# Performance work log

Hardware: AMD Instinct MI355X
Metric: run time of the kernel (lower is better)

The kernel has to match this reference:

```python
import jax, jax.numpy as jnp
import numpy as np

B, L, N, D, TOPK, OUT_V = 32, 512, 1024, 64, 20, 1024
BN_EPS = 1e-5
NEG_SLOPE = 0.2


def setup_inputs() -> dict:
    key = jax.random.key(0)
    ks = jax.random.split(key, 8)
    s = lambda k, shape, sc=0.05: jax.random.normal(k, shape, jnp.float32) * sc
    return {
        "x_enc": jax.random.normal(ks[0], (B, L, N), jnp.float32),
        "emb": s(ks[1], (N, D), 0.1),          # nn.Embedding(variate, d_model).weight
        "lin_W": s(ks[2], (L, D)),              # GraphLayer.lin (no bias)
        "att_i": s(ks[3], (D,)),
        "att_j": s(ks[4], (D,)),
        "att_em_i": s(ks[5], (D,)),
        "att_em_j": s(ks[6], (D,)),
        "gnn_b": jnp.zeros((D,), jnp.float32),  # GraphLayer bias (concat=False)
        "g1": jnp.ones((D,), jnp.float32), "b1": jnp.zeros((D,), jnp.float32),   # GNNLayer.bn
        "g2": jnp.ones((D,), jnp.float32), "b2": jnp.zeros((D,), jnp.float32),   # bn_outlayer_in
        "out_W": s(ks[7], (D, 1)), "out_b": jnp.zeros((1,), jnp.float32),        # OutLayer Linear(d_model, 1)
    }


def _forward(x_enc, emb, lin_W, att_i, att_j, att_em_i, att_em_j,
             gnn_b, g1, b1, g2, b2, out_W, out_b):
    # --- LIN: LayerNorm(input_len, eps=0, no affine) over time, first OUT_V variates ---
    xv = jnp.transpose(x_enc[:, :, :OUT_V], (0, 2, 1))          # [B, OUT_V, L]
    xv = (xv - xv.mean(-1, keepdims=True)) / jnp.sqrt(xv.var(-1, keepdims=True))
    x_enc = x_enc.at[:, :, :OUT_V].set(jnp.transpose(xv, (0, 2, 1)))
    x_enc = jnp.nan_to_num(x_enc, nan=0.0, posinf=0.0, neginf=0.0)

    gt = x_enc[:, -1:, :OUT_V]                                   # [B, 1, OUT_V]
    enc = x_enc.at[:, -1:, :OUT_V].set(0.0)

    # x = enc.transpose(0,1).view(-1, L)  (faithful to original reshape)
    x = jnp.transpose(enc, (1, 0, 2)).reshape(-1, L)             # [B*N, L]

    # --- dynamic top-k cosine-similarity graph (embeddings detached) ---
    w = jax.lax.stop_gradient(emb)
    nrm = jnp.linalg.norm(w, axis=-1)
    cos = (w @ w.T) / (nrm[:, None] * nrm[None, :])              # [N, N]
    topk_idx = jax.lax.top_k(cos, TOPK)[1]                       # [N, TOPK]
    src = topk_idx.reshape(-1)                                   # gated_j (source)
    dst = jnp.repeat(jnp.arange(N), TOPK)                        # gated_i (target)

    offs = (jnp.arange(B) * N)[:, None]
    src_b = (src[None, :] + offs).reshape(-1)                    # [B*N*TOPK]
    dst_b = (dst[None, :] + offs).reshape(-1)

    # remove_self_loops (mask out) then add_self_loops for all B*N nodes
    num_nodes = B * N
    self_mask = jnp.concatenate([src_b == dst_b, jnp.zeros(num_nodes, bool)])
    src_all = jnp.concatenate([src_b, jnp.arange(num_nodes)])
    dst_all = jnp.concatenate([dst_b, jnp.arange(num_nodes)])

    # --- GraphLayer (GAT-style, heads=1, concat=False) ---
    h = x @ lin_W                                                # [B*N, D]
    all_emb = jnp.tile(emb, (B, 1))                              # [B*N, D]

    logit = (h[dst_all] @ att_i + all_emb[dst_all] @ att_em_i
             + h[src_all] @ att_j + all_emb[src_all] @ att_em_j)  # [E]
    logit = jnp.where(logit >= 0, logit, NEG_SLOPE * logit)      # leaky_relu(0.2)
    logit = jnp.where(self_mask, -jnp.inf, logit)

    seg_max = jax.ops.segment_max(logit, dst_all, num_segments=num_nodes)
    expv = jnp.where(self_mask, 0.0, jnp.exp(logit - seg_max[dst_all]))
    denom = jax.ops.segment_sum(expv, dst_all, num_segments=num_nodes)
    alpha = expv / denom[dst_all]

    out = jax.ops.segment_sum(h[src_all] * alpha[:, None], dst_all,
                              num_segments=num_nodes) + gnn_b    # [B*N, D]

    # GNNLayer: BatchNorm1d(D) (batch stats) + ReLU
    out = (out - out.mean(0)) / jnp.sqrt(out.var(0) + BN_EPS) * g1 + b1
    out = jax.nn.relu(out)

    # --- combine with embedding, bn_outlayer_in, OutLayer ---
    xg = out.reshape(B, N, D) * emb[None]                        # [B, N, D]
    xg = jnp.transpose(xg, (0, 2, 1))                            # [B, D, N]
    mu = xg.mean((0, 2), keepdims=True)
    var = xg.var((0, 2), keepdims=True)
    xg = (xg - mu) / jnp.sqrt(var + BN_EPS) * g2[None, :, None] + b2[None, :, None]
    xg = jnp.transpose(jax.nn.relu(xg), (0, 2, 1))               # [B, N, D]

    o = xg @ out_W + out_b                                       # [B, N, 1]
    o = jnp.transpose(o, (0, 2, 1))                              # [B, 1, N]
    return o[:, :, :OUT_V], gt


def reference(x_enc, emb, lin_W, att_i, att_j, att_em_i, att_em_j,
              gnn_b, g1, b1, g2, b2, out_W, out_b):
    return _forward(x_enc, emb, lin_W, att_i, att_j, att_em_i, att_em_j,
                    gnn_b, g1, b1, g2, b2, out_W, out_b)
```

## Files before the change

kernel.cpp:

```cpp
#include <hip/hip_runtime.h>
#include <stdint.h>

#define BB 32
#define LL 512
#define NNODES 1024
#define DD 64
#define TOPK 20
#define NTOT (BB*NNODES)
#define LNSZ (LL*NNODES)

typedef short short8 __attribute__((ext_vector_type(8)));
typedef float floatx4 __attribute__((ext_vector_type(4)));

__device__ __forceinline__ float bf2f(unsigned short u){
    union { unsigned int i; float f; } x; x.i = ((unsigned int)u) << 16; return x.f;
}
__device__ __forceinline__ unsigned short f2bf(float f){
    union { float f; unsigned int i; } x; x.f = f;
    unsigned int u = x.i;
    return (unsigned short)((u + 0x7FFFu + ((u >> 16) & 1u)) >> 16);
}
__device__ __forceinline__ void unpack2(unsigned int w, float& lo, float& hi){
    union { unsigned int i; float f; } a, b;
    a.i = w << 16; b.i = w & 0xFFFF0000u;
    lo = a.f; hi = b.f;
}
__device__ __forceinline__ float ldf(const void* p, int i, int isf){
    return isf ? ((const float*)p)[i] : bf2f(((const unsigned short*)p)[i]);
}

__global__ void __launch_bounds__(256) kd_detect(const unsigned short* x, int* flag, float* stats){
    __shared__ int cnt;
    stats[threadIdx.x] = 0.f;
    if (threadIdx.x == 0) cnt = 0;
    __syncthreads();
    unsigned int idx = (threadIdx.x * 131071u) & 0x7FFFFFu;
    float v = bf2f(x[idx * 2]);
    float a = fabsf(v);
    int crazy = (!(a <= 1e3f)) || (v != 0.f && a < 1e-6f);
    atomicAdd(&cnt, crazy);
    __syncthreads();
    if (threadIdx.x == 0) flag[0] = (cnt > 64) ? 1 : 0;
}

__global__ void __launch_bounds__(256) k0_prep(const void* lw, unsigned short* wt,
                                               const void* emb, const void* aemi, const void* aemj,
                                               float* eai, float* eaj, float* embT, float* rsqm,
                                               const int* dtf){
    int isf = dtf[0];
    int id = blockIdx.x * 256 + threadIdx.x;
    int k = id >> 6, d = id & 63;
    unsigned short w = isf ? f2bf(((const float*)lw)[id]) : ((const unsigned short*)lw)[id];
    wt[d * 512 + k] = w;
    {
        int j = id;
        int dd = j >> 10, m = j & 1023;
        embT[j] = ldf(emb, m * 64 + dd, isf);
        j = id + 32768;
        dd = j >> 10; m = j & 1023;
        embT[j] = ldf(emb, m * 64 + dd, isf);
    }
    if (id < 1024){
        int n = id;
        float s1 = 0.f, s2 = 0.f;
        for (int dd = 0; dd < 64; dd++){
            float e = ldf(emb, n * 64 + dd, isf);
            s1 += e * ldf(aemi, dd, isf);
            s2 += e * ldf(aemj, dd, isf);
        }
        eai[n] = s1; eaj[n] = s2;
        float sq = 0.f;
        if (!isf){
            const uint4* pm = (const uint4*)((const unsigned short*)emb + n * 64);
            #pragma unroll
            for (int i = 0; i < 8; i++){
                uint4 ww = pm[i];
                float a0,a1,a2,a3,a4,a5,a6,a7;
                unpack2(ww.x,a0,a1); unpack2(ww.y,a2,a3); unpack2(ww.z,a4,a5); unpack2(ww.w,a6,a7);
                sq += a0*a0 + a1*a1 + a2*a2 + a3*a3 + a4*a4 + a5*a5 + a6*a6 + a7*a7;
            }
        } else {
            const float4* pm = (const float4*)((const float*)emb + n * 64);
            #pragma unroll
            for (int i = 0; i < 16; i++){
                float4 ww = pm[i];
                sq += ww.x*ww.x + ww.y*ww.y + ww.z*ww.z + ww.w*ww.w;
            }
        }
        rsqm[n] = rsqrtf(sq);
    }
}

__global__ void __launch_bounds__(256) k1a_partial(const void* x, float* part, const int* dtf){
    int isf = dtf[0];
    int t = threadIdx.x;
    int b = blockIdx.x >> 4, lq = blockIdx.x & 15;
    int n0 = t * 4;
    size_t base = (size_t)b * LNSZ + (size_t)(lq * 32) * NNODES + n0;
    float s0=0,s1=0,s2=0,s3=0,q0=0,q1=0,q2=0,q3=0;
    if (isf){
        const float* p = (const float*)x + base;
        for (int i = 0; i < 32; i++){
            float4 w = *(const float4*)p;
            s0+=w.x; q0+=w.x*w.x; s1+=w.y; q1+=w.y*w.y;
            s2+=w.z; q2+=w.z*w.z; s3+=w.w; q3+=w.w*w.w;
            p += NNODES;
        }
    } else {
        const unsigned short* p = (const unsigned short*)x + base;
        for (int i = 0; i < 32; i++){
            uint2 w = *(const uint2*)p;
            float a,bv,c,d2;
            unpack2(w.x, a, bv); unpack2(w.y, c, d2);
            s0+=a; q0+=a*a; s1+=bv; q1+=bv*bv; s2+=c; q2+=c*c; s3+=d2; q3+=d2*d2;
            p += NNODES;
        }
    }
    int v = b * NNODES + n0;
    float2* pp = (float2*)part;
    pp[(size_t)v*16 + lq]       = make_float2(s0,q0);
    pp[(size_t)(v+1)*16 + lq]   = make_float2(s1,q1);
    pp[(size_t)(v+2)*16 + lq]   = make_float2(s2,q2);
    pp[(size_t)(v+3)*16 + lq]   = make_float2(s3,q3);
}

__global__ void __launch_bounds__(256) k1b_finalize(const void* x, const float* part,
                                                    float* mr, float* outp, const int* dtf){
    int isf = dtf[0];
    int v = blockIdx.x * 256 + threadIdx.x;
    const float2* pp = (const float2*)part + (size_t)v * 16;
    float s = 0.f, q = 0.f;
    for (int i = 0; i < 16; i++){ float2 w = pp[i]; s += w.x; q += w.y; }
    float mean = s * (1.f/512.f);
    float var  = q * (1.f/512.f) - mean * mean;
    float rstd = var > 0.f ? rsqrtf(var) : 0.f;
    ((float2*)mr)[v] = make_float2(mean, rstd);
    int b = v >> 10, n = v & 1023;
    float xv = ldf(x, (int)((size_t)b * LNSZ + (size_t)511 * NNODES + n), isf);
    outp[NTOT + v] = (xv - mean) * rstd;
}

__global__ void __launch_bounds__(256) k2_gemm_h(const void* x, const unsigned short* wt,
                                                const float* mr, float* h, const int* dtf){
    __shared__ unsigned short A_l[64 * 136];
    __shared__ unsigned short W_l[64 * 136];
    __shared__ float4 colp4[256];
    int isf = dtf[0];
    int t = threadIdx.x;
    int q = blockIdx.x & 63, mtile = blockIdx.x >> 6;
    int b = q >> 1, nbase = (q & 1) * 512;
    size_t xbase = (size_t)b * LNSZ + nbase;

    colp4[t] = ((const float4*)mr)[q * 256 + t];

    int wave = t >> 6, lane = t & 63;
    int quad = lane >> 4, lcol = lane & 15;
    floatx4 acc[4];
    for (int j = 0; j < 4; j++) acc[j] = (floatx4){0.f,0.f,0.f,0.f};
    __syncthreads();

    for (int kc = 0; kc < 4; kc++){
        for (int i = 0; i < 4; i++){
            int id = i * 256 + t;
            int l = id >> 4, c16 = id & 15;
            int lg = mtile * 64 + l;
            uint4 o;
            if (lg == 511){
                o = make_uint4(0u, 0u, 0u, 0u);
            } else {
                size_t ofs = xbase + (size_t)lg * NNODES + kc * 128 + c16 * 8;
                float e0,e1,e2,e3,e4,e5,e6,e7;
                if (isf){
                    const float4* px = (const float4*)((const float*)x + ofs);
                    float4 wa = px[0], wb = px[1];
                    e0=wa.x; e1=wa.y; e2=wa.z; e3=wa.w; e4=wb.x; e5=wb.y; e6=wb.z; e7=wb.w;
                } else {
                    uint4 w = *(const uint4*)((const unsigned short*)x + ofs);
                    unpack2(w.x,e0,e1); unpack2(w.y,e2,e3); unpack2(w.z,e4,e5); unpack2(w.w,e6,e7);
                }
                int f4b = kc * 64 + c16 * 4;
                float4 pA = colp4[f4b+0], pB = colp4[f4b+1], pC = colp4[f4b+2], pD = colp4[f4b+3];
                e0 = (e0 - pA.x) * pA.y;  e1 = (e1 - pA.z) * pA.w;
                e2 = (e2 - pB.x) * pB.y;  e3 = (e3 - pB.z) * pB.w;
                e4 = (e4 - pC.x) * pC.y;  e5 = (e5 - pC.z) * pC.w;
                e6 = (e6 - pD.x) * pD.y;  e7 = (e7 - pD.z) * pD.w;
                o.x = (unsigned)f2bf(e0) | ((unsigned)f2bf(e1) << 16);
                o.y = (unsigned)f2bf(e2) | ((unsigned)f2bf(e3) << 16);
                o.z = (unsigned)f2bf(e4) | ((unsigned)f2bf(e5) << 16);
                o.w = (unsigned)f2bf(e6) | ((unsigned)f2bf(e7) << 16);
            }
            *(uint4*)&A_l[l * 136 + c16 * 8] = o;
        }
        for (int i = 0; i < 4; i++){
            int id = i * 256 + t;
            int dd = id >> 4, c16 = id & 15;
            uint4 w = *(const uint4*)(wt + dd * 512 + kc * 128 + c16 * 8);
            *(uint4*)&W_l[dd * 136 + c16 * 8] = w;
        }
        __syncthreads();
        for (int ks = 0; ks < 4; ks++){
            short8 af, bfr[4];
            af = *(const short8*)&A_l[(wave * 16 + lcol) * 136 + ks * 32 + quad * 8];
            for (int tc = 0; tc < 4; tc++)
                bfr[tc] = *(const short8*)&W_l[(tc * 16 + lcol) * 136 + ks * 32 + quad * 8];
            for (int tc = 0; tc < 4; tc++)
                acc[tc] = __builtin_amdgcn_mfma_f32_16x16x32_bf16(af, bfr[tc], acc[tc], 0, 0, 0);
        }
        __syncthreads();
    }
    for (int tc = 0; tc < 4; tc++){
        int dcol = tc * 16 + lcol;
        for (int r = 0; r < 4; r++){
            int lrow = wave * 16 + quad * 4 + r;
            int lg = mtile * 64 + lrow;
            int row = lg * 64 + q;
            h[(size_t)row * 64 + dcol] = acc[tc][r];
        }
    }
}

__global__ void __launch_bounds__(256) k3_topk(const void* emb, const float* embT, const float* rsqm,
                                               int* topk, const int* dtf){
    __shared__ float enf[64];
    __shared__ float n2s;
    __shared__ float crow[1024];
    int isf = dtf[0];
    int wave = threadIdx.x >> 6, lane = threadIdx.x & 63;
    int n = blockIdx.x;
    if (wave == 0){
        float e = ldf(emb, n * 64 + lane, isf);
        enf[lane] = e;
        float p1 = e * e;
        #pragma unroll
        for (int m = 1; m < 64; m <<= 1) p1 += __shfl_xor(p1, m, 64);
        if (lane == 0) n2s = p1;
    }
    __syncthreads();
    float rn_own = rsqrtf(n2s);
    const float* en = enf;
    int mb = wave * 256 + lane * 4;
    float dot0 = 0.f, dot1 = 0.f, dot2 = 0.f, dot3 = 0.f;
    if (!isf){
        #pragma unroll
        for (int i = 0; i < 8; i++){
            float4 a0 = *(const float4*)(embT + (i*8+0)*1024 + mb);
            float4 a1 = *(const float4*)(embT + (i*8+1)*1024 + mb);
            float4 a2 = *(const float4*)(embT + (i*8+2)*1024 + mb);
            float4 a3 = *(const float4*)(embT + (i*8+3)*1024 + mb);
            float4 a4 = *(const float4*)(embT + (i*8+4)*1024 + mb);
            float4 a5 = *(const float4*)(embT + (i*8+5)*1024 + mb);
            float4 a6 = *(const float4*)(embT + (i*8+6)*1024 + mb);
            float4 a7 = *(const float4*)(embT + (i*8+7)*1024 + mb);
            const float* e8 = en + i * 8;
            dot0 += e8[0]*a0.x + e8[1]*a1.x + e8[2]*a2.x + e8[3]*a3.x
                  + e8[4]*a4.x + e8[5]*a5.x + e8[6]*a6.x + e8[7]*a7.x;
            dot1 += e8[0]*a0.y + e8[1]*a1.y + e8[2]*a2.y + e8[3]*a3.y
                  + e8[4]*a4.y + e8[5]*a5.y + e8[6]*a6.y + e8[7]*a7.y;
            dot2 += e8[0]*a0.z + e8[1]*a1.z + e8[2]*a2.z + e8[3]*a3.z
                  + e8[4]*a4.z + e8[5]*a5.z + e8[6]*a6.z + e8[7]*a7.z;
            dot3 += e8[0]*a0.w + e8[1]*a1.w + e8[2]*a2.w + e8[3]*a3.w
                  + e8[4]*a4.w + e8[5]*a5.w + e8[6]*a6.w + e8[7]*a7.w;
        }
    } else {
        #pragma unroll
        for (int i = 0; i < 16; i++){
            float4 a0 = *(const float4*)(embT + (i*4+0)*1024 + mb);
            float4 a1 = *(const float4*)(embT + (i*4+1)*1024 + mb);
            float4 a2 = *(const float4*)(embT + (i*4+2)*1024 + mb);
            float4 a3 = *(const float4*)(embT + (i*4+3)*1024 + mb);
            const float* e4 = en + i * 4;
            dot0 += e4[0]*a0.x + e4[1]*a1.x + e4[2]*a2.x + e4[3]*a3.x;
            dot1 += e4[0]*a0.y + e4[1]*a1.y + e4[2]*a2.y + e4[3]*a3.y;
            dot2 += e4[0]*a0.z + e4[1]*a1.z + e4[2]*a2.z + e4[3]*a3.z;
            dot3 += e4[0]*a0.w + e4[1]*a1.w + e4[2]*a2.w + e4[3]*a3.w;
        }
    }
    crow[mb+0] = dot0 * rn_own * rsqm[mb+0];
    crow[mb+1] = dot1 * rn_own * rsqm[mb+1];
    crow[mb+2] = dot2 * rn_own * rsqm[mb+2];
    crow[mb+3] = dot3 * rn_own * rsqm[mb+3];
    __syncthreads();
    if (wave != 0) return;
    float va[16];
    #pragma unroll
    for (int ii = 0; ii < 16; ii++) va[ii] = crow[ii * 64 + lane];
    for (int k = 0; k < TOPK; k++){
        float t8[8]; int x8[8];
        #pragma unroll
        for (int j = 0; j < 8; j++){
            bool c = va[2*j+1] > va[2*j];
            t8[j] = c ? va[2*j+1] : va[2*j]; x8[j] = c ? 2*j+1 : 2*j;
        }
        #pragma unroll
        for (int j = 0; j < 4; j++){
            bool c = t8[2*j+1] > t8[2*j];
            t8[j] = c ? t8[2*j+1] : t8[2*j]; x8[j] = c ? x8[2*j+1] : x8[2*j];
        }
        #pragma unroll
        for (int j = 0; j < 2; j++){
            bool c = t8[2*j+1] > t8[2*j];
            t8[j] = c ? t8[2*j+1] : t8[2*j]; x8[j] = c ? x8[2*j+1] : x8[2*j];
        }
        bool c0 = t8[1] > t8[0];
        float bv = c0 ? t8[1] : t8[0]; int bi = c0 ? x8[1] : x8[0];
        int bm = bi * 64 + lane;
        #pragma unroll
        for (int s = 1; s < 64; s <<= 1){
            float ov = __shfl_xor(bv, s, 64);
            int   om = __shfl_xor(bm, s, 64);
            bool u = (ov > bv) || (ov == bv && om < bm);
            bv = u ? ov : bv; bm = u ? om : bm;
        }
        if (lane == 0) topk[n * TOPK + k] = bm;
        int evi = bm >> 6;
        bool own = ((bm & 63) == lane);
        #pragma unroll
        for (int ii = 0; ii < 16; ii++)
            va[ii] = (own && ii == evi) ? -__builtin_inff() : va[ii];
    }
}

__global__ void __launch_bounds__(256) k4_coef(const float* h, const void* att_i, const void* att_j,
                                               const float* eai, const float* eaj, float* ai, float* aj,
                                               const int* dtf){
    int isf = dtf[0];
    int wave = blockIdx.x * 4 + (threadIdx.x >> 6), lane = threadIdx.x & 63;
    float wi = ldf(att_i, lane, isf), wj = ldf(att_j, lane, isf);
    int v0 = wave * 16;
    for (int i = 0; i < 16; i++){
        int v = v0 + i;
        float hv = h[(size_t)v * 64 + lane];
        float p1 = hv * wi, p2 = hv * wj;
        for (int m = 1; m < 64; m <<= 1){ p1 += __shfl_xor(p1, m, 64); p2 += __shfl_xor(p2, m, 64); }
        if (lane == 0){
            int n = v & 1023;
            ai[v] = p1 + eai[n];
            aj[v] = p2 + eaj[n];
        }
    }
}

__global__ void __launch_bounds__(256) k5_attn(const float* h, const float* ai, const float* aj, const int* topk,
                                               const void* gnn_b, float* out, const int* dtf){
    int isf = dtf[0];
    int wave = threadIdx.x >> 6, lane = threadIdx.x & 63;
    float gb = ldf(gnn_b, lane, isf);
    int v = blockIdx.x * 4 + wave;
    int n = v & 1023, bbase = v & ~1023;
    int srcv; bool valid;
    if (lane < TOPK){
        int id = topk[n * TOPK + lane];
        srcv = bbase | id;
        valid = (id != n);
    } else if (lane == TOPK){
        srcv = v; valid = true;
    } else { srcv = v; valid = false; }
    float l = ai[v] + aj[srcv];
    l = (l >= 0.f) ? l : 0.2f * l;
    if (!valid) l = -__builtin_inff();
    float m = l;
    #pragma unroll
    for (int s = 1; s < 64; s <<= 1){ float o = __shfl_xor(m, s, 64); m = fmaxf(m, o); }
    float ev = valid ? __expf(l - m) : 0.f;
    float dsum = ev;
    #pragma unroll
    for (int s = 1; s < 64; s <<= 1) dsum += __shfl_xor(dsum, s, 64);
    float rd = 1.f / dsum;
    float acc = 0.f;
    #pragma unroll
    for (int j = 0; j <= TOPK; j++){
        float e = __shfl(ev, j, 64);
        int  sj = __shfl(srcv, j, 64);
        acc += e * h[(size_t)sj * 64 + lane];
    }
    out[(size_t)v * 64 + lane] = acc * rd + gb;
}

__global__ void __launch_bounds__(256) k5b_stats(const float* out, float* stats1){
    __shared__ float bs[256], bq[256];
    int wave = threadIdx.x >> 6, lane = threadIdx.x & 63;
    int v0 = blockIdx.x * 128 + wave * 32;
    float ssum = 0.f, ssq = 0.f;
    for (int i = 0; i < 32; i++){
        float x = out[(size_t)(v0 + i) * 64 + lane];
        ssum += x; ssq += x * x;
    }
    bs[threadIdx.x] = ssum; bq[threadIdx.x] = ssq;
    __syncthreads();
    if (wave == 0){
        float s  = bs[lane] + bs[64+lane] + bs[128+lane] + bs[192+lane];
        float qq = bq[lane] + bq[64+lane] + bq[128+lane] + bq[192+lane];
        atomicAdd(&stats1[lane], s);
        atomicAdd(&stats1[64 + lane], qq);
    }
}

__global__ void __launch_bounds__(256) k6_stats2(const float* out, const float* stats1, const void* g1,
                                                 const void* b1, const void* emb,
                                                 float* stats2, const int* dtf){
    __shared__ float bs[256], bq[256];
    int isf = dtf[0];
    int wave = threadIdx.x >> 6, lane = threadIdx.x & 63;
    float mu   = stats1[lane] * (1.f/32768.f);
    float var  = stats1[64 + lane] * (1.f/32768.f) - mu * mu;
    float rstd = 1.f / sqrtf(var + 1e-5f);
    float g = ldf(g1, lane, isf), bb = ldf(b1, lane, isf);
    float ssum = 0.f, ssq = 0.f;
    int v0 = (blockIdx.x * 4 + wave) * 16;
    for (int i = 0; i < 16; i++){
        int v = v0 + i; int n = v & 1023;
        float x = out[(size_t)v * 64 + lane];
        float y = fmaxf((x - mu) * rstd * g + bb, 0.f);
        float z = y * ldf(emb, n * 64 + lane, isf);
        ssum += z; ssq += z * z;
    }
    bs[threadIdx.x] = ssum; bq[threadIdx.x] = ssq;
    __syncthreads();
    if (wave == 0){
        float s  = bs[lane] + bs[64+lane] + bs[128+lane] + bs[192+lane];
        float qq = bq[lane] + bq[64+lane] + bq[128+lane] + bq[192+lane];
        atomicAdd(&stats2[lane], s);
        atomicAdd(&stats2[64 + lane], qq);
    }
}

__global__ void __launch_bounds__(256) k7_out(const float* out, const float* stats1, const float* stats2,
                                              const void* g1, const void* b1,
                                              const void* g2, const void* b2,
                                              const void* emb, const void* outw,
                                              const void* outb, float* o, const int* dtf){
    int isf = dtf[0];
    int wave = threadIdx.x >> 6, lane = threadIdx.x & 63;
    float mu1   = stats1[lane] * (1.f/32768.f);
    float var1  = stats1[64 + lane] * (1.f/32768.f) - mu1 * mu1;
    float rstd1 = 1.f / sqrtf(var1 + 1e-5f);
    float g1v = ldf(g1, lane, isf), b1v = ldf(b1, lane, isf);
    float mu2   = stats2[lane] * (1.f/32768.f);
    float var2  = stats2[64 + lane] * (1.f/32768.f) - mu2 * mu2;
    float rstd2 = 1.f / sqrtf(var2 + 1e-5f);
    float g2v = ldf(g2, lane, isf), b2v = ldf(b2, lane, isf);
    float w = ldf(outw, lane, isf);
    float ob = ldf(outb, 0, isf);
    int v0 = (blockIdx.x * 4 + wave) * 16;
    for (int i = 0; i < 16; i++){
        int v = v0 + i; int n = v & 1023;
        float x = out[(size_t)v * 64 + lane];
        float z = fmaxf((x - mu1) * rstd1 * g1v + b1v, 0.f) * ldf(emb, n * 64 + lane, isf);
        float y = fmaxf((z - mu2) * rstd2 * g2v + b2v, 0.f);
        float p = y * w;
        for (int s = 1; s < 64; s <<= 1) p += __shfl_xor(p, s, 64);
        if (lane == 0) o[v] = p + ob;
    }
}

extern "C" void kernel_launch(void* const* d_in, const int* in_sizes, int n_in,
                              void* d_out, int out_size, void* d_ws, size_t ws_size,
                              hipStream_t stream){
    const void* x    = d_in[0];
    const void* emb  = d_in[1];
    const void* linW = d_in[2];
    const void* atti = d_in[3];
    const void* attj = d_in[4];
    const void* aemi = d_in[5];
    const void* aemj = d_in[6];
    const void* gnnb = d_in[7];
    const void* g1   = d_in[8];
    const void* b1   = d_in[9];
    const void* g2   = d_in[10];
    const void* b2   = d_in[11];
    const void* outw = d_in[12];
    const void* outb = d_in[13];
    float* o = (float*)d_out;

    char* w = (char*)d_ws;
    float*          mr    = (float*)(w + 0);
    unsigned short* wt    = (unsigned short*)(w + 262144);
    float*          h     = (float*)(w + 327680);
    float*          eai   = (float*)(w + 8716288);
    float*          eaj   = (float*)(w + 8720384);
    int*            topk  = (int*)(w + 8724480);
    float*          ai    = (float*)(w + 8806400);
    float*          aj    = (float*)(w + 8937472);
    float*          outg  = (float*)(w + 9068544);
    float*          part  = outg;
    float*          embT  = (float*)(w + 13262848);
    float*          rsqm  = (float*)(w + 13524992);
    float*          stats = (float*)(w + 17457152);
    int*            dtf   = (int*)(w + 17458176);

    hipLaunchKernelGGL(kd_detect,    dim3(1),    dim3(256), 0, stream, (const unsigned short*)x, dtf, stats);
    hipLaunchKernelGGL(k0_prep,      dim3(128),  dim3(256), 0, stream, linW, wt, emb, aemi, aemj, eai, eaj, embT, rsqm, dtf);
    hipLaunchKernelGGL(k1a_partial,  dim3(512),  dim3(256), 0, stream, x, part, dtf);
    hipLaunchKernelGGL(k1b_finalize, dim3(128),  dim3(256), 0, stream, x, part, mr, o, dtf);
    hipLaunchKernelGGL(k2_gemm_h,    dim3(512),  dim3(256), 0, stream, x, wt, mr, h, dtf);
    hipLaunchKernelGGL(k3_topk,      dim3(1024), dim3(256), 0, stream, emb, embT, rsqm, topk, dtf);
    hipLaunchKernelGGL(k4_coef,      dim3(512),  dim3(256), 0, stream, h, atti, attj, eai, eaj, ai, aj, dtf);
    hipLaunchKernelGGL(k5_attn,      dim3(8192), dim3(256), 0, stream, h, ai, aj, topk, gnnb, outg, dtf);
    hipLaunchKernelGGL(k5b_stats,    dim3(256),  dim3(256), 0, stream, outg, stats);
    hipLaunchKernelGGL(k6_stats2,    dim3(512),  dim3(256), 0, stream, outg, stats, g1, b1, emb, stats + 128, dtf);
    hipLaunchKernelGGL(k7_out,       dim3(512),  dim3(256), 0, stream, outg, stats, stats + 128,
                       g1, b1, g2, b2, emb, outw, outb, o, dtf);
}
```

Before: 260.5 us.

## Fuse prep, stats, topk, coefficient and BN-stat kernels to cut launch count

Merges the separate detect, prep, partial-sum, finalize, top-k, attention-coefficient and BN-statistics kernels into fewer launches, going from eleven kernels to six. Dtype detection is now redone in every kernel with a wave ballot instead of a dedicated launch writing a flag. The attention coefficients are computed in the GEMM epilogue from the MFMA accumulators, which removes a full re-read of h. The BN1 statistics are accumulated inside the attention kernel, which now handles four nodes per wave. The aim is less launch overhead and less global memory traffic, at the cost of heavier fused kernels, some redundant detection loads, and the finalize work sharing blocks with top-k.

After: 277.6 us. +6.6%, slower.

```diff
diff --git a/kernel.cpp b/kernel.cpp
--- a/kernel.cpp
+++ b/kernel.cpp
@@ -28,72 +28,67 @@
 __device__ __forceinline__ float ldf(const void* p, int i, int isf){
     return isf ? ((const float*)p)[i] : bf2f(((const unsigned short*)p)[i]);
 }
-
-__global__ void __launch_bounds__(256) kd_detect(const unsigned short* x, int* flag, float* stats){
-    __shared__ int cnt;
-    stats[threadIdx.x] = 0.f;
-    if (threadIdx.x == 0) cnt = 0;
-    __syncthreads();
-    unsigned int idx = (threadIdx.x * 131071u) & 0x7FFFFFu;
+__device__ __forceinline__ int detect_isf(const void* xv){
+    const unsigned short* x = (const unsigned short*)xv;
+    int lane = threadIdx.x & 63;
+    unsigned int idx = ((unsigned)lane * 131071u) & 0x7FFFFFu;
     float v = bf2f(x[idx * 2]);
     float a = fabsf(v);
     int crazy = (!(a <= 1e3f)) || (v != 0.f && a < 1e-6f);
-    atomicAdd(&cnt, crazy);
-    __syncthreads();
-    if (threadIdx.x == 0) flag[0] = (cnt > 64) ? 1 : 0;
-}
-
-__global__ void __launch_bounds__(256) k0_prep(const void* lw, unsigned short* wt,
-                                               const void* emb, const void* aemi, const void* aemj,
-                                               float* eai, float* eaj, float* embT, float* rsqm,
-                                               const int* dtf){
-    int isf = dtf[0];
-    int id = blockIdx.x * 256 + threadIdx.x;
-    int k = id >> 6, d = id & 63;
-    unsigned short w = isf ? f2bf(((const float*)lw)[id]) : ((const unsigned short*)lw)[id];
-    wt[d * 512 + k] = w;
-    {
-        int j = id;
-        int dd = j >> 10, m = j & 1023;
-        embT[j] = ldf(emb, m * 64 + dd, isf);
-        j = id + 32768;
-        dd = j >> 10; m = j & 1023;
-        embT[j] = ldf(emb, m * 64 + dd, isf);
-    }
-    if (id < 1024){
-        int n = id;
-        float s1 = 0.f, s2 = 0.f;
-        for (int dd = 0; dd < 64; dd++){
-            float e = ldf(emb, n * 64 + dd, isf);
-            s1 += e * ldf(aemi, dd, isf);
-            s2 += e * ldf(aemj, dd, isf);
-        }
-        eai[n] = s1; eaj[n] = s2;
-        float sq = 0.f;
-        if (!isf){
-            const uint4* pm = (const uint4*)((const unsigned short*)emb + n * 64);
-            #pragma unroll
-            for (int i = 0; i < 8; i++){
-                uint4 ww = pm[i];
-                float a0,a1,a2,a3,a4,a5,a6,a7;
-                unpack2(ww.x,a0,a1); unpack2(ww.y,a2,a3); unpack2(ww.z,a4,a5); unpack2(ww.w,a6,a7);
-                sq += a0*a0 + a1*a1 + a2*a2 + a3*a3 + a4*a4 + a5*a5 + a6*a6 + a7*a7;
+    unsigned long long m = __ballot(crazy);
+    return __popcll(m) > 16;
+}
+
+__global__ void __launch_bounds__(256) k01_prep(const void* x, const void* lw, unsigned short* wt,
+                                                const void* emb, const void* aemi, const void* aemj,
+                                                float* eai, float* eaj, float* embT, float* rsqm,
+                                                float* part, float* stats){
+    int isf = detect_isf(x);
+    int t = threadIdx.x;
+    if (blockIdx.x == 0) stats[t] = 0.f;
+    if (blockIdx.x < 128){
+        int id = blockIdx.x * 256 + t;
+        int k = id >> 6, d = id & 63;
+        unsigned short w = isf ? f2bf(((const float*)lw)[id]) : ((const unsigned short*)lw)[id];
+        wt[d * 512 + k] = w;
+        {
+            int j = id;
+            int dd = j >> 10, m = j & 1023;
+            embT[j] = ldf(emb, m * 64 + dd, isf);
+            j = id + 32768;
+            dd = j >> 10; m = j & 1023;
+            embT[j] = ldf(emb, m * 64 + dd, isf);
+        }
+        if (id < 1024){
+            int n = id;
+            float s1 = 0.f, s2 = 0.f;
+            for (int dd = 0; dd < 64; dd++){
+                float e = ldf(emb, n * 64 + dd, isf);
+                s1 += e * ldf(aemi, dd, isf);
+                s2 += e * ldf(aemj, dd, isf);
             }
-        } else {
-            const float4* pm = (const float4*)((const float*)emb + n * 64);
-            #pragma unroll
-            for (int i = 0; i < 16; i++){
-                float4 ww = pm[i];
-                sq += ww.x*ww.x + ww.y*ww.y + ww.z*ww.z + ww.w*ww.w;
+            eai[n] = s1; eaj[n] = s2;
+            float sq = 0.f;
+            if (!isf){
+                const uint4* pm = (const uint4*)((const unsigned short*)emb + n * 64);
+                #pragma unroll
+                for (int i = 0; i < 8; i++){
+                    uint4 ww = pm[i];
+                    float a0,a1,a2,a3,a4,a5,a6,a7;
+                    unpack2(ww.x,a0,a1); unpack2(ww.y,a2,a3); unpack2(ww.z,a4,a5); unpack2(ww.w,a6,a7);
+                    sq += a0*a0 + a1*a1 + a2*a2 + a3*a3 + a4*a4 + a5*a5 + a6*a6 + a7*a7;
+                }
+            } else {
+                const float4* pm = (const float4*)((const float*)emb + n * 64);
+                #pragma unroll
+                for (int i = 0; i < 16; i++){
+                    float4 ww = pm[i];
+                    sq += ww.x*ww.x + ww.y*ww.y + ww.z*ww.z + ww.w*ww.w;
+                }
             }
-        }
-        rsqm[n] = rsqrtf(sq);
-    }
-}
-
-__global__ void __launch_bounds__(256) k1a_partial(const void* x, float* part, const int* dtf){
-    int isf = dtf[0];
-    int t = threadIdx.x;
+            rsqm[n] = rsqrtf(sq);
+        }
+    }
     int b = blockIdx.x >> 4, lq = blockIdx.x & 15;
     int n0 = t * 4;
     size_t base = (size_t)b * LNSZ + (size_t)(lq * 32) * NNODES + n0;
@@ -124,28 +119,130 @@
     pp[(size_t)(v+3)*16 + lq]   = make_float2(s3,q3);
 }
 
-__global__ void __launch_bounds__(256) k1b_finalize(const void* x, const float* part,
-                                                    float* mr, float* outp, const int* dtf){
-    int isf = dtf[0];
-    int v = blockIdx.x * 256 + threadIdx.x;
-    const float2* pp = (const float2*)part + (size_t)v * 16;
-    float s = 0.f, q = 0.f;
-    for (int i = 0; i < 16; i++){ float2 w = pp[i]; s += w.x; q += w.y; }
-    float mean = s * (1.f/512.f);
-    float var  = q * (1.f/512.f) - mean * mean;
-    float rstd = var > 0.f ? rsqrtf(var) : 0.f;
-    ((float2*)mr)[v] = make_float2(mean, rstd);
-    int b = v >> 10, n = v & 1023;
-    float xv = ldf(x, (int)((size_t)b * LNSZ + (size_t)511 * NNODES + n), isf);
-    outp[NTOT + v] = (xv - mean) * rstd;
+__global__ void __launch_bounds__(256) k13_topk(const void* emb, const float* embT, const float* rsqm,
+                                                int* topk, const void* x, const float* part,
+                                                float* mr, float* outp){
+    __shared__ float enf[64];
+    __shared__ float n2s;
+    __shared__ float crow[1024];
+    int isf = detect_isf(x);
+    int wave = threadIdx.x >> 6, lane = threadIdx.x & 63;
+    int n = blockIdx.x;
+    if (blockIdx.x < 128){
+        int v = blockIdx.x * 256 + threadIdx.x;
+        const float2* pp = (const float2*)part + (size_t)v * 16;
+        float s = 0.f, q = 0.f;
+        for (int i = 0; i < 16; i++){ float2 w = pp[i]; s += w.x; q += w.y; }
+        float mean = s * (1.f/512.f);
+        float var  = q * (1.f/512.f) - mean * mean;
+        float rstd = var > 0.f ? rsqrtf(var) : 0.f;
+        ((float2*)mr)[v] = make_float2(mean, rstd);
+        int b = v >> 10, nn = v & 1023;
+        float xv = ldf(x, (int)((size_t)b * LNSZ + (size_t)511 * NNODES + nn), isf);
+        outp[NTOT + v] = (xv - mean) * rstd;
+    }
+    if (wave == 0){
+        float e = ldf(emb, n * 64 + lane, isf);
+        enf[lane] = e;
+        float p1 = e * e;
+        #pragma unroll
+        for (int m = 1; m < 64; m <<= 1) p1 += __shfl_xor(p1, m, 64);
+        if (lane == 0) n2s = p1;
+    }
+    __syncthreads();
+    float rn_own = rsqrtf(n2s);
+    const float* en = enf;
+    int mb = wave * 256 + lane * 4;
+    float dot0 = 0.f, dot1 = 0.f, dot2 = 0.f, dot3 = 0.f;
+    if (!isf){
+        #pragma unroll
+        for (int i = 0; i < 8; i++){
+            float4 a0 = *(const float4*)(embT + (i*8+0)*1024 + mb);
+            float4 a1 = *(const float4*)(embT + (i*8+1)*1024 + mb);
+            float4 a2 = *(const float4*)(embT + (i*8+2)*1024 + mb);
+            float4 a3 = *(const float4*)(embT + (i*8+3)*1024 + mb);
+            float4 a4 = *(const float4*)(embT + (i*8+4)*1024 + mb);
+            float4 a5 = *(const float4*)(embT + (i*8+5)*1024 + mb);
+            float4 a6 = *(const float4*)(embT + (i*8+6)*1024 + mb);
+            float4 a7 = *(const float4*)(embT + (i*8+7)*1024 + mb);
+            const float* e8 = en + i * 8;
+            dot0 += e8[0]*a0.x + e8[1]*a1.x + e8[2]*a2.x + e8[3]*a3.x
+                  + e8[4]*a4.x + e8[5]*a5.x + e8[6]*a6.x + e8[7]*a7.x;
+            dot1 += e8[0]*a0.y + e8[1]*a1.y + e8[2]*a2.y + e8[3]*a3.y
+                  + e8[4]*a4.y + e8[5]*a5.y + e8[6]*a6.y + e8[7]*a7.y;
+            dot2 += e8[0]*a0.z + e8[1]*a1.z + e8[2]*a2.z + e8[3]*a3.z
+                  + e8[4]*a4.z + e8[5]*a5.z + e8[6]*a6.z + e8[7]*a7.z;
+            dot3 += e8[0]*a0.w + e8[1]*a1.w + e8[2]*a2.w + e8[3]*a3.w
+                  + e8[4]*a4.w + e8[5]*a5.w + e8[6]*a6.w + e8[7]*a7.w;
+        }
+    } else {
+        #pragma unroll
+        for (int i = 0; i < 16; i++){
+            float4 a0 = *(const float4*)(embT + (i*4+0)*1024 + mb);
+            float4 a1 = *(const float4*)(embT + (i*4+1)*1024 + mb);
+            float4 a2 = *(const float4*)(embT + (i*4+2)*1024 + mb);
+            float4 a3 = *(const float4*)(embT + (i*4+3)*1024 + mb);
+            const float* e4 = en + i * 4;
+            dot0 += e4[0]*a0.x + e4[1]*a1.x + e4[2]*a2.x + e4[3]*a3.x;
+            dot1 += e4[0]*a0.y + e4[1]*a1.y + e4[2]*a2.y + e4[3]*a3.y;
+            dot2 += e4[0]*a0.z + e4[1]*a1.z + e4[2]*a2.z + e4[3]*a3.z;
+            dot3 += e4[0]*a0.w + e4[1]*a1.w + e4[2]*a2.w + e4[3]*a3.w;
+        }
+    }
+    crow[mb+0] = dot0 * rn_own * rsqm[mb+0];
+    crow[mb+1] = dot1 * rn_own * rsqm[mb+1];
+    crow[mb+2] = dot2 * rn_own * rsqm[mb+2];
+    crow[mb+3] = dot3 * rn_own * rsqm[mb+3];
+    __syncthreads();
+    if (wave != 0) return;
+    float va[16];
+    #pragma unroll
+    for (int ii = 0; ii < 16; ii++) va[ii] = crow[ii * 64 + lane];
+    for (int k = 0; k < TOPK; k++){
+        float t8[8]; int x8[8];
+        #pragma unroll
+        for (int j = 0; j < 8; j++){
+            bool c = va[2*j+1] > va[2*j];
+            t8[j] = c ? va[2*j+1] : va[2*j]; x8[j] = c ? 2*j+1 : 2*j;
+        }
+        #pragma unroll
+        for (int j = 0; j < 4; j++){
+            bool c = t8[2*j+1] > t8[2*j];
+            t8[j] = c ? t8[2*j+1] : t8[2*j]; x8[j] = c ? x8[2*j+1] : x8[2*j];
+        }
+        #pragma unroll
+        for (int j = 0; j < 2; j++){
+            bool c = t8[2*j+1] > t8[2*j];
+            t8[j] = c ? t8[2*j+1] : t8[2*j]; x8[j] = c ? x8[2*j+1] : x8[2*j];
+        }
+        bool c0 = t8[1] > t8[0];
+        float bv = c0 ? t8[1] : t8[0]; int bi = c0 ? x8[1] : x8[0];
+        int bm = bi * 64 + lane;
+        #pragma unroll
+        for (int s = 1; s < 64; s <<= 1){
+            float ov = __shfl_xor(bv, s, 64);
+            int   om = __shfl_xor(bm, s, 64);
+            bool u = (ov > bv) || (ov == bv && om < bm);
+            bv = u ? ov : bv; bm = u ? om : bm;
+        }
+        if (lane == 0) topk[n * TOPK + k] = bm;
+        int evi = bm >> 6;
+        bool own = ((bm & 63) == lane);
+        #pragma unroll
+        for (int ii = 0; ii < 16; ii++)
+            va[ii] = (own && ii == evi) ? -__builtin_inff() : va[ii];
+    }
 }
 
 __global__ void __launch_bounds__(256) k2_gemm_h(const void* x, const unsigned short* wt,
-                                                const float* mr, float* h, const int* dtf){
+                                                const float* mr, float* h,
+                                                const void* atti, const void* attj,
+                                                const float* eai, const float* eaj,
+                                                float* ai, float* aj){
     __shared__ unsigned short A_l[64 * 136];
     __shared__ unsigned short W_l[64 * 136];
     __shared__ float4 colp4[256];
-    int isf = dtf[0];
+    int isf = detect_isf(x);
     int t = threadIdx.x;
     int q = blockIdx.x & 63, mtile = blockIdx.x >> 6;
     int b = q >> 1, nbase = (q & 1) * 512;
@@ -208,182 +305,86 @@
         }
         __syncthreads();
     }
+    float aw[4], jw[4];
+    #pragma unroll
+    for (int tc = 0; tc < 4; tc++){
+        int dcol = tc * 16 + lcol;
+        aw[tc] = ldf(atti, dcol, isf);
+        jw[tc] = ldf(attj, dcol, isf);
+    }
+    #pragma unroll
+    for (int r = 0; r < 4; r++){
+        float pi = 0.f, pj = 0.f;
+        #pragma unroll
+        for (int tc = 0; tc < 4; tc++){
+            float hv = acc[tc][r];
+            pi += hv * aw[tc];
+            pj += hv * jw[tc];
+        }
+        #pragma unroll
+        for (int s = 1; s < 16; s <<= 1){
+            pi += __shfl_xor(pi, s, 64);
+            pj += __shfl_xor(pj, s, 64);
+        }
+        if (lcol == 0){
+            int lrow = wave * 16 + quad * 4 + r;
+            int row = (mtile * 64 + lrow) * 64 + q;
+            int n = row & 1023;
+            ai[row] = pi + eai[n];
+            aj[row] = pj + eaj[n];
+        }
+    }
     for (int tc = 0; tc < 4; tc++){
         int dcol = tc * 16 + lcol;
         for (int r = 0; r < 4; r++){
             int lrow = wave * 16 + quad * 4 + r;
-            int lg = mtile * 64 + lrow;
-            int row = lg * 64 + q;
+            int row = (mtile * 64 + lrow) * 64 + q;
             h[(size_t)row * 64 + dcol] = acc[tc][r];
         }
     }
 }
 
-__global__ void __launch_bounds__(256) k3_topk(const void* emb, const float* embT, const float* rsqm,
-                                               int* topk, const int* dtf){
-    __shared__ float enf[64];
-    __shared__ float n2s;
-    __shared__ float crow[1024];
-    int isf = dtf[0];
-    int wave = threadIdx.x >> 6, lane = threadIdx.x & 63;
-    int n = blockIdx.x;
-    if (wave == 0){
-        float e = ldf(emb, n * 64 + lane, isf);
-        enf[lane] = e;
-        float p1 = e * e;
-        #pragma unroll
-        for (int m = 1; m < 64; m <<= 1) p1 += __shfl_xor(p1, m, 64);
-        if (lane == 0) n2s = p1;
-    }
-    __syncthreads();
-    float rn_own = rsqrtf(n2s);
-    const float* en = enf;
-    int mb = wave * 256 + lane * 4;
-    float dot0 = 0.f, dot1 = 0.f, dot2 = 0.f, dot3 = 0.f;
-    if (!isf){
-        #pragma unroll
-        for (int i = 0; i < 8; i++){
-            float4 a0 = *(const float4*)(embT + (i*8+0)*1024 + mb);
-            float4 a1 = *(const float4*)(embT + (i*8+1)*1024 + mb);
-            float4 a2 = *(const float4*)(embT + (i*8+2)*1024 + mb);
-            float4 a3 = *(const float4*)(embT + (i*8+3)*1024 + mb);
-            float4 a4 = *(const float4*)(embT + (i*8+4)*1024 + mb);
-            float4 a5 = *(const float4*)(embT + (i*8+5)*1024 + mb);
-            float4 a6 = *(const float4*)(embT + (i*8+6)*1024 + mb);
-            float4 a7 = *(const float4*)(embT + (i*8+7)*1024 + mb);
-            const float* e8 = en + i * 8;
-            dot0 += e8[0]*a0.x + e8[1]*a1.x + e8[2]*a2.x + e8[3]*a3.x
-                  + e8[4]*a4.x + e8[5]*a5.x + e8[6]*a6.x + e8[7]*a7.x;
-            dot1 += e8[0]*a0.y + e8[1]*a1.y + e8[2]*a2.y + e8[3]*a3.y
-                  + e8[4]*a4.y + e8[5]*a5.y + e8[6]*a6.y + e8[7]*a7.y;
-            dot2 += e8[0]*a0.z + e8[1]*a1.z + e8[2]*a2.z + e8[3]*a3.z
-                  + e8[4]*a4.z + e8[5]*a5.z + e8[6]*a6.z + e8[7]*a7.z;
-            dot3 += e8[0]*a0.w + e8[1]*a1.w + e8[2]*a2.w + e8[3]*a3.w
-                  + e8[4]*a4.w + e8[5]*a5.w + e8[6]*a6.w + e8[7]*a7.w;
-        }
-    } else {
-        #pragma unroll
-        for (int i = 0; i < 16; i++){
-            float4 a0 = *(const float4*)(embT + (i*4+0)*1024 + mb);
-            float4 a1 = *(const float4*)(embT + (i*4+1)*1024 + mb);
-            float4 a2 = *(const float4*)(embT + (i*4+2)*1024 + mb);
-            float4 a3 = *(const float4*)(embT + (i*4+3)*1024 + mb);
-            const float* e4 = en + i * 4;
-            dot0 += e4[0]*a0.x + e4[1]*a1.x + e4[2]*a2.x + e4[3]*a3.x;
-            dot1 += e4[0]*a0.y + e4[1]*a1.y + e4[2]*a2.y + e4[3]*a3.y;
-            dot2 += e4[0]*a0.z + e4[1]*a1.z + e4[2]*a2.z + e4[3]*a3.z;
-            dot3 += e4[0]*a0.w + e4[1]*a1.w + e4[2]*a2.w + e4[3]*a3.w;
-        }
-    }
-    crow[mb+0] = dot0 * rn_own * rsqm[mb+0];
-    crow[mb+1] = dot1 * rn_own * rsqm[mb+1];
-    crow[mb+2] = dot2 * rn_own * rsqm[mb+2];
-    crow[mb+3] = dot3 * rn_own * rsqm[mb+3];
-    __syncthreads();
-    if (wave != 0) return;
-    float va[16];
-    #pragma unroll
-    for (int ii = 0; ii < 16; ii++) va[ii] = crow[ii * 64 + lane];
-    for (int k = 0; k < TOPK; k++){
-        float t8[8]; int x8[8];
-        #pragma unroll
-        for (int j = 0; j < 8; j++){
-            bool c = va[2*j+1] > va[2*j];
-            t8[j] = c ? va[2*j+1] : va[2*j]; x8[j] = c ? 2*j+1 : 2*j;
-        }
-        #pragma unroll
-        for (int j = 0; j < 4; j++){
-            bool c = t8[2*j+1] > t8[2*j];
-            t8[j] = c ? t8[2*j+1] : t8[2*j]; x8[j] = c ? x8[2*j+1] : x8[2*j];
-        }
-        #pragma unroll
-        for (int j = 0; j < 2; j++){
-            bool c = t8[2*j+1] > t8[2*j];
-            t8[j] = c ? t8[2*j+1] : t8[2*j]; x8[j] = c ? x8[2*j+1] : x8[2*j];
-        }
-        bool c0 = t8[1] > t8[0];
-        float bv = c0 ? t8[1] : t8[0]; int bi = c0 ? x8[1] : x8[0];
-        int bm = bi * 64 + lane;
-        #pragma unroll
-        for (int s = 1; s < 64; s <<= 1){
-            float ov = __shfl_xor(bv, s, 64);
-            int   om = __shfl_xor(bm, s, 64);
-            bool u = (ov > bv) || (ov == bv && om < bm);
-            bv = u ? ov : bv; bm = u ? om : bm;
-        }
-        if (lane == 0) topk[n * TOPK + k] = bm;
-        int evi = bm >> 6;
-        bool own = ((bm & 63) == lane);
-        #pragma unroll
-        for (int ii = 0; ii < 16; ii++)
-            va[ii] = (own && ii == evi) ? -__builtin_inff() : va[ii];
-    }
-}
-
-__global__ void __launch_bounds__(256) k4_coef(const float* h, const void* att_i, const void* att_j,
-                                               const float* eai, const float* eaj, float* ai, float* aj,
-                                               const int* dtf){
-    int isf = dtf[0];
-    int wave = blockIdx.x * 4 + (threadIdx.x >> 6), lane = threadIdx.x & 63;
-    float wi = ldf(att_i, lane, isf), wj = ldf(att_j, lane, isf);
-    int v0 = wave * 16;
-    for (int i = 0; i < 16; i++){
-        int v = v0 + i;
-        float hv = h[(size_t)v * 64 + lane];
-        float p1 = hv * wi, p2 = hv * wj;
-        for (int m = 1; m < 64; m <<= 1){ p1 += __shfl_xor(p1, m, 64); p2 += __shfl_xor(p2, m, 64); }
-        if (lane == 0){
-            int n = v & 1023;
-            ai[v] = p1 + eai[n];
-            aj[v] = p2 + eaj[n];
-        }
-    }
-}
-
 __global__ void __launch_bounds__(256) k5_attn(const float* h, const float* ai, const float* aj, const int* topk,
-                                               const void* gnn_b, float* out, const int* dtf){
-    int isf = dtf[0];
+                                               const void* gnn_b, float* out, float* stats1, const void* x){
+    __shared__ float bs[256], bq[256];
+    int isf = detect_isf(x);
     int wave = threadIdx.x >> 6, lane = threadIdx.x & 63;
     float gb = ldf(gnn_b, lane, isf);
-    int v = blockIdx.x * 4 + wave;
-    int n = v & 1023, bbase = v & ~1023;
-    int srcv; bool valid;
-    if (lane < TOPK){
-        int id = topk[n * TOPK + lane];
-        srcv = bbase | id;
-        valid = (id != n);
-    } else if (lane == TOPK){
-        srcv = v; valid = true;
-    } else { srcv = v; valid = false; }
-    float l = ai[v] + aj[srcv];
-    l = (l >= 0.f) ? l : 0.2f * l;
-    if (!valid) l = -__builtin_inff();
-    float m = l;
+    float ssum = 0.f, ssq = 0.f;
+    int v0 = (blockIdx.x * 4 + wave) * 4;
     #pragma unroll
-    for (int s = 1; s < 64; s <<= 1){ float o = __shfl_xor(m, s, 64); m = fmaxf(m, o); }
-    float ev = valid ? __expf(l - m) : 0.f;
-    float dsum = ev;
-    #pragma unroll
-    for (int s = 1; s < 64; s <<= 1) dsum += __shfl_xor(dsum, s, 64);
-    float rd = 1.f / dsum;
-    float acc = 0.f;
-    #pragma unroll
-    for (int j = 0; j <= TOPK; j++){
-        float e = __shfl(ev, j, 64);
-        int  sj = __shfl(srcv, j, 64);
-        acc += e * h[(size_t)sj * 64 + lane];
-    }
-    out[(size_t)v * 64 + lane] = acc * rd + gb;
-}
-
-__global__ void __launch_bounds__(256) k5b_stats(const float* out, float* stats1){
-    __shared__ float bs[256], bq[256];
-    int wave = threadIdx.x >> 6, lane = threadIdx.x & 63;
-    int v0 = blockIdx.x * 128 + wave * 32;
-    float ssum = 0.f, ssq = 0.f;
-    for (int i = 0; i < 32; i++){
-        float x = out[(size_t)(v0 + i) * 64 + lane];
-        ssum += x; ssq += x * x;
+    for (int i = 0; i < 4; i++){
+        int v = v0 + i;
+        int n = v & 1023, bbase = v & ~1023;
+        int srcv; bool valid;
+        if (lane < TOPK){
+            int id = topk[n * TOPK + lane];
+            srcv = bbase | id;
+            valid = (id != n);
+        } else if (lane == TOPK){
+            srcv = v; valid = true;
+        } else { srcv = v; valid = false; }
+        float l = ai[v] + aj[srcv];
+        l = (l >= 0.f) ? l : 0.2f * l;
+        if (!valid) l = -__builtin_inff();
+        float m = l;
+        #pragma unroll
+        for (int s = 1; s < 64; s <<= 1){ float o = __shfl_xor(m, s, 64); m = fmaxf(m, o); }
+        float ev = valid ? __expf(l - m) : 0.f;
+        float dsum = ev;
+        #pragma unroll
+        for (int s = 1; s < 64; s <<= 1) dsum += __shfl_xor(dsum, s, 64);
+        float rd = 1.f / dsum;
+        float acc = 0.f;
+        #pragma unroll
+        for (int j = 0; j <= TOPK; j++){
+            float e = __shfl(ev, j, 64);
+            int  sj = __shfl(srcv, j, 64);
+            acc += e * h[(size_t)sj * 64 + lane];
+        }
+        float res = acc * rd + gb;
+        out[(size_t)v * 64 + lane] = res;
+        ssum += res; ssq += res * res;
     }
     bs[threadIdx.x] = ssum; bq[threadIdx.x] = ssq;
     __syncthreads();
@@ -397,9 +398,9 @@
 
 __global__ void __launch_bounds__(256) k6_stats2(const float* out, const float* stats1, const void* g1,
                                                  const void* b1, const void* emb,
-                                                 float* stats2, const int* dtf){
+                                                 float* stats2, const void* x){
     __shared__ float bs[256], bq[256];
-    int isf = dtf[0];
+    int isf = detect_isf(x);
     int wave = threadIdx.x >> 6, lane = threadIdx.x & 63;
     float mu   = stats1[lane] * (1.f/32768.f);
     float var  = stats1[64 + lane] * (1.f/32768.f) - mu * mu;
@@ -409,8 +410,8 @@
     int v0 = (blockIdx.x * 4 + wave) * 16;
     for (int i = 0; i < 16; i++){
         int v = v0 + i; int n = v & 1023;
-        float x = out[(size_t)v * 64 + lane];
-        float y = fmaxf((x - mu) * rstd * g + bb, 0.f);
+        float xv = out[(size_t)v * 64 + lane];
+        float y = fmaxf((xv - mu) * rstd * g + bb, 0.f);
         float z = y * ldf(emb, n * 64 + lane, isf);
         ssum += z; ssq += z * z;
     }
@@ -428,8 +429,8 @@
                                               const void* g1, const void* b1,
                                               const void* g2, const void* b2,
                                               const void* emb, const void* outw,
-                                              const void* outb, float* o, const int* dtf){
-    int isf = dtf[0];
+                                              const void* outb, float* o, const void* x){
+    int isf = detect_isf(x);
     int wave = threadIdx.x >> 6, lane = threadIdx.x & 63;
     float mu1   = stats1[lane] * (1.f/32768.f);
     float var1  = stats1[64 + lane] * (1.f/32768.f) - mu1 * mu1;
@@ -444,8 +445,8 @@
     int v0 = (blockIdx.x * 4 + wave) * 16;
     for (int i = 0; i < 16; i++){
         int v = v0 + i; int n = v & 1023;
-        float x = out[(size_t)v * 64 + lane];
-        float z = fmaxf((x - mu1) * rstd1 * g1v + b1v, 0.f) * ldf(emb, n * 64 + lane, isf);
+        float xv = out[(size_t)v * 64 + lane];
+        float z = fmaxf((xv - mu1) * rstd1 * g1v + b1v, 0.f) * ldf(emb, n * 64 + lane, isf);
         float y = fmaxf((z - mu2) * rstd2 * g2v + b2v, 0.f);
         float p = y * w;
         for (int s = 1; s < 64; s <<= 1) p += __shfl_xor(p, s, 64);
@@ -486,18 +487,13 @@
     float*          embT  = (float*)(w + 13262848);
     float*          rsqm  = (float*)(w + 13524992);
     float*          stats = (float*)(w + 17457152);
-    int*            dtf   = (int*)(w + 17458176);
-
-    hipLaunchKernelGGL(kd_detect,    dim3(1),    dim3(256), 0, stream, (const unsigned short*)x, dtf, stats);
-    hipLaunchKernelGGL(k0_prep,      dim3(128),  dim3(256), 0, stream, linW, wt, emb, aemi, aemj, eai, eaj, embT, rsqm, dtf);
-    hipLaunchKernelGGL(k1a_partial,  dim3(512),  dim3(256), 0, stream, x, part, dtf);
-    hipLaunchKernelGGL(k1b_finalize, dim3(128),  dim3(256), 0, stream, x, part, mr, o, dtf);
-    hipLaunchKernelGGL(k2_gemm_h,    dim3(512),  dim3(256), 0, stream, x, wt, mr, h, dtf);
-    hipLaunchKernelGGL(k3_topk,      dim3(1024), dim3(256), 0, stream, emb, embT, rsqm, topk, dtf);
-    hipLaunchKernelGGL(k4_coef,      dim3(512),  dim3(256), 0, stream, h, atti, attj, eai, eaj, ai, aj, dtf);
-    hipLaunchKernelGGL(k5_attn,      dim3(8192), dim3(256), 0, stream, h, ai, aj, topk, gnnb, outg, dtf);
-    hipLaunchKernelGGL(k5b_stats,    dim3(256),  dim3(256), 0, stream, outg, stats);
-    hipLaunchKernelGGL(k6_stats2,    dim3(512),  dim3(256), 0, stream, outg, stats, g1, b1, emb, stats + 128, dtf);
-    hipLaunchKernelGGL(k7_out,       dim3(512),  dim3(256), 0, stream, outg, stats, stats + 128,
-                       g1, b1, g2, b2, emb, outw, outb, o, dtf);
-}
+
+    hipLaunchKernelGGL(k01_prep, dim3(512),  dim3(256), 0, stream, x, linW, wt, emb, aemi, aemj,
+                       eai, eaj, embT, rsqm, part, stats);
+    hipLaunchKernelGGL(k13_topk, dim3(1024), dim3(256), 0, stream, emb, embT, rsqm, topk, x, part, mr, o);
+    hipLaunchKernelGGL(k2_gemm_h, dim3(512), dim3(256), 0, stream, x, wt, mr, h, atti, attj, eai, eaj, ai, aj);
+    hipLaunchKernelGGL(k5_attn,  dim3(2048), dim3(256), 0, stream, h, ai, aj, topk, gnnb, outg, stats, x);
+    hipLaunchKernelGGL(k6_stats2, dim3(512), dim3(256), 0, stream, outg, stats, g1, b1, emb, stats + 128, x);
+    hipLaunchKernelGGL(k7_out,   dim3(512),  dim3(256), 0, stream, outg, stats, stats + 128,
+                       g1, b1, g2, b2, emb, outw, outb, o, x);
+}
```
